# Performance work log

Hardware: AMD Instinct MI355X
Metric: run time of the kernel (lower is better)

## Reference

```python
import jax, jax.numpy as jnp
import numpy as np

DIM = 256
DH = 64            # dim_head
HEADS = DIM // DH  # 4
WH = WW = 8        # window size
EPS = 1e-5


def setup_inputs() -> dict:
    key = jax.random.key(0)
    k1, k2, k3 = jax.random.split(key, 3)
    x = jax.random.normal(k1, (4, DIM, 256, 256), dtype=jnp.float32)
    Wqkv = jax.random.normal(k2, (3 * DIM, DIM), dtype=jnp.float32) * (DIM ** -0.5)
    Wout = jax.random.normal(k3, (DIM, DIM), dtype=jnp.float32) * (DIM ** -0.5)
    gamma = jnp.ones((DIM,), dtype=jnp.float32)
    beta = jnp.zeros((DIM,), dtype=jnp.float32)
    return {"x": x, "gamma": gamma, "beta": beta, "Wqkv": Wqkv, "Wout": Wout}


def _to_windows(t, B, nh, nw):
    # (B, nh*WH, nw*WW, HEADS*DH) -> (B, nh, nw, HEADS, WH*WW, DH)
    t = t.reshape(B, nh, WH, nw, WW, HEADS, DH)
    t = t.transpose(0, 1, 3, 5, 2, 4, 6)
    return t.reshape(B, nh, nw, HEADS, WH * WW, DH)


def reference(x, gamma, beta, Wqkv, Wout):
    B, C, H, W = x.shape
    residual = x
    xh = x.transpose(0, 2, 3, 1)  # (B, H, W, C)
    # LayerNorm over channel dim
    mu = jnp.mean(xh, axis=-1, keepdims=True)
    var = jnp.mean(jnp.square(xh - mu), axis=-1, keepdims=True)
    xn = (xh - mu) * jax.lax.rsqrt(var + EPS) * gamma + beta
    nh, nw = H // WH, W // WW
    qkv = jnp.einsum('bhwc,fc->bhwf', xn, Wqkv)  # (B,H,W,3C)
    q, k, v = jnp.split(qkv, 3, axis=-1)
    q = _to_windows(q, B, nh, nw)
    k = _to_windows(k, B, nh, nw)
    v = _to_windows(v, B, nh, nw)
    scale = DH ** -0.5
    scores = jnp.einsum('bnmhqd,bnmhkd->bnmhqk', q, k) * scale  # 64x64 per window
    attn = jax.nn.softmax(scores, axis=-1)
    o = jnp.einsum('bnmhqk,bnmhkd->bnmhqd', attn, v)
    # merge windows back: (B,nh,nw,HEADS,WH*WW,DH) -> (B,H,W,C)
    o = o.reshape(B, nh, nw, HEADS, WH, WW, DH)
    o = o.transpose(0, 1, 4, 2, 5, 3, 6).reshape(B, H, W, C)
    o = jnp.einsum('bhwc,fc->bhwf', o, Wout)
    return o.transpose(0, 3, 1, 2) + residual
```

## Files before the change

kernel.cpp:

```cpp
#include <hip/hip_runtime.h>
#include <hip/hip_bf16.h>

typedef __attribute__((ext_vector_type(8))) short short8;
typedef __attribute__((ext_vector_type(4))) float floatx4;
typedef __attribute__((ext_vector_type(2))) float floatx2;
typedef __attribute__((ext_vector_type(4))) unsigned short ushort4v;

#define DEVI static __device__ __forceinline__

DEVI unsigned short f2bf(float f) {
  union { __hip_bfloat16 b; unsigned short u; } v;
  v.b = __float2bfloat16(f);
  return v.u;
}
DEVI float bf2f(unsigned short h) { return __uint_as_float(((unsigned int)h) << 16); }

DEVI int ridx2(int c, int t) { return c * 128 + (t ^ ((c & 7) << 3)); }
DEVI int xnaddr(int row, int chunk) { return row * 256 + (((chunk) ^ (row & 7)) << 3); }

DEVI short8 wpfrag(const unsigned short* __restrict__ wbf, int rb, int kc, int lane) {
  return *(const short8*)&wbf[(((size_t)rb * 8 + kc) * 64 + lane) * 8];
}

__global__ void wconv(const float* __restrict__ wqkv, const float* __restrict__ wout,
                      unsigned short* __restrict__ wbf) {
  int cl = blockIdx.x * 256 + threadIdx.x;
  int lane = cl & 63;
  int rbkc = cl >> 6;
  int kc = rbkc & 7;
  int rb = rbkc >> 3;
  int g = lane >> 4, l15 = lane & 15;
  const float* src = (rb < 48) ? wqkv : wout;
  int row = (rb < 48) ? rb * 16 + l15 : (rb - 48) * 16 + l15;
#pragma unroll
  for (int h = 0; h < 2; ++h)
#pragma unroll
    for (int e = 0; e < 4; ++e)
      wbf[(size_t)cl * 8 + h * 4 + e] = f2bf(src[row * 256 + kc * 32 + h * 16 + g * 4 + e]);
}

__global__ __launch_bounds__(512, 2) void k1a_qkv(
    const float* __restrict__ x, const float* __restrict__ gamma,
    const float* __restrict__ beta, const unsigned short* __restrict__ wbf,
    unsigned short* __restrict__ frag) {
  __shared__ __align__(16) unsigned short sx[128 * 256];
  __shared__ floatx2 psum[4][128];

  const int tid = threadIdx.x;
  const int lane = tid & 63;
  const int wv = tid >> 6;
  const int g = lane >> 4;
  const int l15 = lane & 15;

  const int id = ((blockIdx.x & 7) << 8) + (blockIdx.x >> 3);
  const int b = id >> 9;
  const int wy = (id >> 4) & 31;
  const int wxp = id & 15;
  const size_t xbase = ((size_t)b << 24) + (size_t)(wy * 8) * 256 + (size_t)(wxp * 16);

#pragma unroll
  for (int it = 0; it < 16; ++it) {
    int s = it * 512 + tid;
    int c = s >> 5, i = (s >> 2) & 7, j4 = s & 3;
    floatx4 v = *(const floatx4*)(x + xbase + (size_t)c * 65536 + i * 256 + j4 * 4);
    ushort4v u;
    u.x = f2bf(v.x); u.y = f2bf(v.y); u.z = f2bf(v.z); u.w = f2bf(v.w);
    *(ushort4v*)&sx[ridx2(c, i * 16 + j4 * 4)] = u;
  }
  __syncthreads();

  const int t = tid & 127;
  const int q = tid >> 7;
  unsigned int xr[32];
  float s1 = 0.f, s2 = 0.f;
#pragma unroll
  for (int cc = 0; cc < 32; ++cc) {
    unsigned int u0 = sx[ridx2(q * 64 + 2 * cc, t)];
    unsigned int u1 = sx[ridx2(q * 64 + 2 * cc + 1, t)];
    xr[cc] = u0 | (u1 << 16);
    float a = __uint_as_float(u0 << 16);
    float c2 = __uint_as_float(u1 << 16);
    s1 += a + c2;
    s2 = fmaf(a, a, s2); s2 = fmaf(c2, c2, s2);
  }
  { floatx2 p; p.x = s1; p.y = s2; psum[q][t] = p; }
  __syncthreads();

  float S1 = 0.f, S2 = 0.f;
#pragma unroll
  for (int p = 0; p < 4; ++p) { floatx2 pp = psum[p][t]; S1 += pp.x; S2 += pp.y; }
  const float mu = S1 * (1.f / 256.f);
  const float rstd = rsqrtf(S2 * (1.f / 256.f) - mu * mu + 1e-5f);

#pragma unroll
  for (int kk = 0; kk < 2; ++kk) {
    int kc = q * 2 + kk;
#pragma unroll
    for (int gc = 0; gc < 4; ++gc) {
      short8 s8;
#pragma unroll
      for (int hf = 0; hf < 2; ++hf)
#pragma unroll
        for (int e = 0; e < 4; ++e) {
          int lc = kk * 32 + hf * 16 + gc * 4 + e;
          int c = q * 64 + lc;
          unsigned int u = xr[lc >> 1];
          float xv = __uint_as_float((lc & 1) ? (u & 0xffff0000u) : (u << 16));
          float val = (xv - mu) * rstd * gamma[c] + beta[c];
          s8[hf * 4 + e] = (short)f2bf(val);
        }
      *(short8*)&sx[xnaddr(t, kc * 4 + gc)] = s8;
    }
  }
  __syncthreads();

  auto ldsfrag = [&](int row, int kc) -> short8 {
    return *(const short8*)&sx[xnaddr(row, kc * 4 + g)];
  };

  const int head = wv >> 1;
  const int win = wv & 1;
  auto srow = [&](int tl) { return (((tl) >> 3) << 4) + win * 8 + ((tl) & 7); };

  unsigned short* fr = frag + ((size_t)(id * 8 + wv) * 24) * 512 + (size_t)lane * 8;

#pragma unroll
  for (int qk = 0; qk < 2; ++qk) {
    floatx4 acc[4][4] = {};
    const int rbq = qk * 16 + head * 4;
#pragma unroll
    for (int kh = 0; kh < 2; ++kh) {
      short8 wreg[4][4];
#pragma unroll
      for (int kk = 0; kk < 4; ++kk)
#pragma unroll
        for (int mt = 0; mt < 4; ++mt)
          wreg[kk][mt] = wpfrag(wbf, rbq + mt, kh * 4 + kk, lane);
#pragma unroll
      for (int kk = 0; kk < 4; ++kk) {
        int kc = kh * 4 + kk;
        short8 Bv[4];
#pragma unroll
        for (int nt = 0; nt < 4; ++nt) Bv[nt] = ldsfrag(srow(nt * 16 + l15), kc);
#pragma unroll
        for (int mt = 0; mt < 4; ++mt)
#pragma unroll
          for (int nt = 0; nt < 4; ++nt)
            acc[mt][nt] = __builtin_amdgcn_mfma_f32_16x16x32_bf16(wreg[kk][mt], Bv[nt], acc[mt][nt], 0, 0, 0);
      }
    }
#pragma unroll
    for (int nt = 0; nt < 4; ++nt)
#pragma unroll
      for (int ks = 0; ks < 2; ++ks) {
        short8 f;
#pragma unroll
        for (int e = 0; e < 4; ++e) {
          f[e]     = (short)f2bf(acc[2 * ks][nt][e]);
          f[4 + e] = (short)f2bf(acc[2 * ks + 1][nt][e]);
        }
        *(short8*)&fr[(size_t)(qk * 8 + nt * 2 + ks) * 512] = f;
      }
  }

  {
    floatx4 acc[4][4] = {};
#pragma unroll
    for (int kh = 0; kh < 2; ++kh) {
      short8 wreg[4][4];
#pragma unroll
      for (int kk = 0; kk < 4; ++kk)
#pragma unroll
        for (int nt = 0; nt < 4; ++nt)
          wreg[kk][nt] = wpfrag(wbf, 32 + head * 4 + nt, kh * 4 + kk, lane);
#pragma unroll
      for (int kk = 0; kk < 4; ++kk) {
        int kc = kh * 4 + kk;
        short8 Av[4];
#pragma unroll
        for (int mt = 0; mt < 4; ++mt) Av[mt] = ldsfrag(srow(mt * 16 + l15), kc);
#pragma unroll
        for (int mt = 0; mt < 4; ++mt)
#pragma unroll
          for (int nt = 0; nt < 4; ++nt)
            acc[mt][nt] = __builtin_amdgcn_mfma_f32_16x16x32_bf16(Av[mt], wreg[kk][nt], acc[mt][nt], 0, 0, 0);
      }
    }
#pragma unroll
    for (int nt = 0; nt < 4; ++nt)
#pragma unroll
      for (int ks = 0; ks < 2; ++ks) {
        short8 f;
#pragma unroll
        for (int e = 0; e < 4; ++e) {
          f[e]     = (short)f2bf(acc[2 * ks][nt][e]);
          f[4 + e] = (short)f2bf(acc[2 * ks + 1][nt][e]);
        }
        *(short8*)&fr[(size_t)(16 + nt * 2 + ks) * 512] = f;
      }
  }
}

__global__ __launch_bounds__(256, 1) void k1b_attn(
    const unsigned short* __restrict__ frag, unsigned short* __restrict__ o_scr) {
  const int tid = threadIdx.x;
  const int lane = tid & 63;
  const int head = tid >> 6;
  const int g = lane >> 4;
  const int l15 = lane & 15;

  const int id = ((blockIdx.x & 7) << 8) + (blockIdx.x >> 3);
  const int b = id >> 9;
  const int wy = (id >> 4) & 31;
  const int wxp = id & 15;

  const float CEXP = 0.125f * 1.44269504088896f;

#pragma unroll 1
  for (int win = 0; win < 2; ++win) {
    const unsigned short* fr =
        frag + ((size_t)(id * 8 + head * 2 + win) * 24) * 512 + (size_t)lane * 8;

    short8 qkf[2][4][2];
#pragma unroll
    for (int qk = 0; qk < 2; ++qk)
#pragma unroll
      for (int nt = 0; nt < 4; ++nt)
#pragma unroll
        for (int ks = 0; ks < 2; ++ks)
          qkf[qk][nt][ks] = *(const short8*)&fr[(size_t)(qk * 8 + nt * 2 + ks) * 512];

    short8 pf[4][2];
#pragma unroll
    for (int nts = 0; nts < 4; ++nts) {
      floatx4 sac[4] = {};
#pragma unroll
      for (int ks = 0; ks < 2; ++ks)
#pragma unroll
        for (int mts = 0; mts < 4; ++mts)
          sac[mts] = __builtin_amdgcn_mfma_f32_16x16x32_bf16(qkf[1][mts][ks], qkf[0][nts][ks], sac[mts], 0, 0, 0);

      float m = sac[0][0];
#pragma unroll
      for (int mts = 0; mts < 4; ++mts)
#pragma unroll
        for (int r = 0; r < 4; ++r) m = fmaxf(m, sac[mts][r]);
      m = fmaxf(m, __shfl_xor(m, 16));
      m = fmaxf(m, __shfl_xor(m, 32));
      float sum = 0.f;
#pragma unroll
      for (int mts = 0; mts < 4; ++mts)
#pragma unroll
        for (int r = 0; r < 4; ++r) {
          float p = __builtin_amdgcn_exp2f((sac[mts][r] - m) * CEXP);
          sac[mts][r] = p;
          sum += p;
        }
      sum += __shfl_xor(sum, 16);
      sum += __shfl_xor(sum, 32);
      float inv = __builtin_amdgcn_rcpf(sum);
#pragma unroll
      for (int ks = 0; ks < 2; ++ks) {
        short8 f;
#pragma unroll
        for (int e = 0; e < 4; ++e) {
          f[e]     = (short)f2bf(sac[2 * ks][e] * inv);
          f[4 + e] = (short)f2bf(sac[2 * ks + 1][e] * inv);
        }
        pf[nts][ks] = f;
      }
    }

    short8 vf[4][2];
#pragma unroll
    for (int nt = 0; nt < 4; ++nt)
#pragma unroll
      for (int ks = 0; ks < 2; ++ks)
        vf[nt][ks] = *(const short8*)&fr[(size_t)(16 + nt * 2 + ks) * 512];

    floatx4 oa2[4][4];
#pragma unroll
    for (int dt = 0; dt < 4; ++dt)
#pragma unroll
      for (int ntq = 0; ntq < 4; ++ntq) oa2[dt][ntq] = floatx4{0.f, 0.f, 0.f, 0.f};
#pragma unroll
    for (int ks = 0; ks < 2; ++ks)
#pragma unroll
      for (int dt = 0; dt < 4; ++dt)
#pragma unroll
        for (int ntq = 0; ntq < 4; ++ntq)
          oa2[dt][ntq] = __builtin_amdgcn_mfma_f32_16x16x32_bf16(vf[dt][ks], pf[ntq][ks], oa2[dt][ntq], 0, 0, 0);

#pragma unroll
    for (int dtp = 0; dtp < 2; ++dtp)
#pragma unroll
      for (int ntq = 0; ntq < 4; ++ntq) {
        int tq = ntq * 16 + l15;
        size_t orow = ((size_t)b * 256 + wy * 8 + (tq >> 3)) * 256 + wxp * 16 + win * 8 + (tq & 7);
        short8 o8;
#pragma unroll
        for (int r = 0; r < 4; ++r) {
          o8[r]     = (short)f2bf(oa2[2 * dtp][ntq][r]);
          o8[4 + r] = (short)f2bf(oa2[2 * dtp + 1][ntq][r]);
        }
        *(short8*)&o_scr[orow * 256 + head * 64 + dtp * 32 + g * 8] = o8;
      }
  }
}

__global__ __launch_bounds__(512, 2) void k2_proj(
    const unsigned short* __restrict__ o_scr, const float* __restrict__ x,
    const unsigned short* __restrict__ wbf, float* __restrict__ out) {
  __shared__ __align__(16) unsigned short sx[128 * 256];

  const int tid = threadIdx.x;
  const int lane = tid & 63;
  const int wv = tid >> 6;
  const int g = lane >> 4;
  const int l15 = lane & 15;

  const int b = blockIdx.x >> 8;
  const int h = blockIdx.x & 255;

  auto ldsfrag = [&](int row, int kc) -> short8 {
    return *(const short8*)&sx[xnaddr(row, kc * 4 + g)];
  };

#pragma unroll
  for (int hf = 0; hf < 2; ++hf) {
    const size_t obase = (((size_t)b * 256 + h) * 256 + hf * 128) * 256;
#pragma unroll
    for (int it = 0; it < 8; ++it) {
      int s = it * 512 + tid;
      int tl = s >> 5, cid = s & 31;
      short8 v = *(const short8*)&o_scr[obase + tl * 256 + cid * 8];
      *(short8*)&sx[tl * 256 + ((cid ^ (tl & 7)) << 3)] = v;
    }
    __syncthreads();

    floatx4 fa[8][2] = {};
#pragma unroll
    for (int kc = 0; kc < 8; ++kc) {
      short8 Atok[8], Bw[2];
#pragma unroll
      for (int nt = 0; nt < 8; ++nt) Atok[nt] = ldsfrag(nt * 16 + l15, kc);
#pragma unroll
      for (int mt = 0; mt < 2; ++mt)
        Bw[mt] = wpfrag(wbf, 48 + wv * 2 + mt, kc, lane);
#pragma unroll
      for (int nt = 0; nt < 8; ++nt)
#pragma unroll
        for (int mt = 0; mt < 2; ++mt)
          fa[nt][mt] = __builtin_amdgcn_mfma_f32_16x16x32_bf16(Atok[nt], Bw[mt], fa[nt][mt], 0, 0, 0);
    }

#pragma unroll
    for (int nt = 0; nt < 8; ++nt)
#pragma unroll
      for (int mt = 0; mt < 2; ++mt) {
        int co = wv * 32 + mt * 16 + l15;
        size_t addr = (((size_t)(b * 256 + co)) << 16) + (size_t)h * 256 +
                      hf * 128 + nt * 16 + 4 * g;
        floatx4 xv = *(const floatx4*)(x + addr);
        floatx4 o;
#pragma unroll
        for (int r = 0; r < 4; ++r) o[r] = fa[nt][mt][r] + xv[r];
        *(floatx4*)(out + addr) = o;
      }
    __syncthreads();
  }
}

__global__ __launch_bounds__(512, 2) void fused_fallback(
    const float* __restrict__ x, const float* __restrict__ gamma,
    const float* __restrict__ beta, const unsigned short* __restrict__ wbf,
    float* __restrict__ out) {
  __shared__ __align__(16) unsigned short sres[256 * 128];
  __shared__ __align__(16) unsigned short sxn[128 * 256];

  const int tid = threadIdx.x;
  const int lane = tid & 63;
  const int wv = tid >> 6;
  const int g = lane >> 4;
  const int l15 = lane & 15;

  const int id = ((blockIdx.x & 7) << 8) + (blockIdx.x >> 3);
  const int b = id >> 9;
  const int wy = (id >> 4) & 31;
  const int wxp = id & 15;
  const size_t xbase = ((size_t)b << 24) + (size_t)(wy * 8) * 256 + (size_t)(wxp * 16);

#pragma unroll
  for (int it = 0; it < 16; ++it) {
    int s = it * 512 + tid;
    int c = s >> 5, i = (s >> 2) & 7, j4 = s & 3;
    floatx4 v = *(const floatx4*)(x + xbase + (size_t)c * 65536 + i * 256 + j4 * 4);
    ushort4v u;
    u.x = f2bf(v.x); u.y = f2bf(v.y); u.z = f2bf(v.z); u.w = f2bf(v.w);
    *(ushort4v*)&sres[ridx2(c, i * 16 + j4 * 4)] = u;
  }
  __syncthreads();

  const int t = tid & 127;
  const int q = tid >> 7;
  float s1 = 0.f, s2 = 0.f;
#pragma unroll 8
  for (int cc = 0; cc < 64; ++cc) {
    float xv = bf2f(sres[ridx2(q * 64 + cc, t)]);
    s1 += xv; s2 += xv * xv;
  }
  { floatx2 p; p.x = s1; p.y = s2; ((floatx2*)sxn)[q * 128 + t] = p; }
  __syncthreads();

  float S1 = 0.f, S2 = 0.f;
#pragma unroll
  for (int p = 0; p < 4; ++p) {
    floatx2 pp = ((const floatx2*)sxn)[p * 128 + t];
    S1 += pp.x; S2 += pp.y;
  }
  const float mu = S1 * (1.f / 256.f);
  const float rstd = rsqrtf(S2 * (1.f / 256.f) - mu * mu + 1e-5f);
  __syncthreads();

#pragma unroll
  for (int kk = 0; kk < 2; ++kk) {
    int kc = q * 2 + kk;
#pragma unroll
    for (int gc = 0; gc < 4; ++gc) {
      short8 s8;
#pragma unroll
      for (int hf = 0; hf < 2; ++hf)
#pragma unroll
        for (int e = 0; e < 4; ++e) {
          int c = kc * 32 + hf * 16 + gc * 4 + e;
          float xv = bf2f(sres[ridx2(c, t)]);
          float val = (xv - mu) * rstd * gamma[c] + beta[c];
          s8[hf * 4 + e] = (short)f2bf(val);
        }
      *(short8*)&sxn[xnaddr(t, kc * 4 + gc)] = s8;
    }
  }
  __syncthreads();

  auto ldsfrag = [&](int row, int kc) -> short8 {
    return *(const short8*)&sxn[xnaddr(row, kc * 4 + g)];
  };

  const int head = wv >> 1;
  const int win = wv & 1;
  auto srow = [&](int tl) { return (((tl) >> 3) << 4) + win * 8 + ((tl) & 7); };

  short8 qkf[2][4][2];
#pragma unroll
  for (int qk = 0; qk < 2; ++qk) {
    floatx4 acc[4][4] = {};
    const int rbq = qk * 16 + head * 4;
#pragma unroll
    for (int kc = 0; kc < 8; ++kc) {
      short8 Bv[4], Av[4];
#pragma unroll
      for (int nt = 0; nt < 4; ++nt) Bv[nt] = ldsfrag(srow(nt * 16 + l15), kc);
#pragma unroll
      for (int mt = 0; mt < 4; ++mt)
        Av[mt] = wpfrag(wbf, rbq + mt, kc, lane);
#pragma unroll
      for (int mt = 0; mt < 4; ++mt)
#pragma unroll
        for (int nt = 0; nt < 4; ++nt)
          acc[mt][nt] = __builtin_amdgcn_mfma_f32_16x16x32_bf16(Av[mt], Bv[nt], acc[mt][nt], 0, 0, 0);
    }
#pragma unroll
    for (int nt = 0; nt < 4; ++nt)
#pragma unroll
      for (int ks = 0; ks < 2; ++ks) {
        short8 f;
#pragma unroll
        for (int e = 0; e < 4; ++e) {
          f[e]     = (short)f2bf(acc[2 * ks][nt][e]);
          f[4 + e] = (short)f2bf(acc[2 * ks + 1][nt][e]);
        }
        qkf[qk][nt][ks] = f;
      }
  }

  floatx4 sa[4][4] = {};
#pragma unroll
  for (int ks = 0; ks < 2; ++ks)
#pragma unroll
    for (int mts = 0; mts < 4; ++mts)
#pragma unroll
      for (int nts = 0; nts < 4; ++nts)
        sa[mts][nts] = __builtin_amdgcn_mfma_f32_16x16x32_bf16(qkf[1][mts][ks], qkf[0][nts][ks], sa[mts][nts], 0, 0, 0);

  short8 pf[4][2];
  const float CEXP = 0.125f * 1.44269504088896f;
#pragma unroll
  for (int nts = 0; nts < 4; ++nts) {
    float m = sa[0][nts][0];
#pragma unroll
    for (int mts = 0; mts < 4; ++mts)
#pragma unroll
      for (int r = 0; r < 4; ++r) m = fmaxf(m, sa[mts][nts][r]);
    m = fmaxf(m, __shfl_xor(m, 16));
    m = fmaxf(m, __shfl_xor(m, 32));
    float sum = 0.f;
#pragma unroll
    for (int mts = 0; mts < 4; ++mts)
#pragma unroll
      for (int r = 0; r < 4; ++r) {
        float p = __builtin_amdgcn_exp2f((sa[mts][nts][r] - m) * CEXP);
        sa[mts][nts][r] = p;
        sum += p;
      }
    sum += __shfl_xor(sum, 16);
    sum += __shfl_xor(sum, 32);
    float inv = __builtin_amdgcn_rcpf(sum);
#pragma unroll
    for (int ks = 0; ks < 2; ++ks) {
      short8 f;
#pragma unroll
      for (int e = 0; e < 4; ++e) {
        f[e]     = (short)f2bf(sa[2 * ks][nts][e] * inv);
        f[4 + e] = (short)f2bf(sa[2 * ks + 1][nts][e] * inv);
      }
      pf[nts][ks] = f;
    }
  }

  short8 vf[4][2];
  {
    floatx4 acc[4][4] = {};
#pragma unroll
    for (int kc = 0; kc < 8; ++kc) {
      short8 Av[4], Bv[4];
#pragma unroll
      for (int mt = 0; mt < 4; ++mt) Av[mt] = ldsfrag(srow(mt * 16 + l15), kc);
#pragma unroll
      for (int nt = 0; nt < 4; ++nt)
        Bv[nt] = wpfrag(wbf, 32 + head * 4 + nt, kc, lane);
#pragma unroll
      for (int mt = 0; mt < 4; ++mt)
#pragma unroll
        for (int nt = 0; nt < 4; ++nt)
          acc[mt][nt] = __builtin_amdgcn_mfma_f32_16x16x32_bf16(Av[mt], Bv[nt], acc[mt][nt], 0, 0, 0);
    }
#pragma unroll
    for (int nt = 0; nt < 4; ++nt)
#pragma unroll
      for (int ks = 0; ks < 2; ++ks) {
        short8 f;
#pragma unroll
        for (int e = 0; e < 4; ++e) {
          f[e]     = (short)f2bf(acc[2 * ks][nt][e]);
          f[4 + e] = (short)f2bf(acc[2 * ks + 1][nt][e]);
        }
        vf[nt][ks] = f;
      }
  }

  floatx4 oa[4][4] = {};
#pragma unroll
  for (int ks = 0; ks < 2; ++ks)
#pragma unroll
    for (int ntq = 0; ntq < 4; ++ntq)
#pragma unroll
      for (int dt = 0; dt < 4; ++dt)
        oa[ntq][dt] = __builtin_amdgcn_mfma_f32_16x16x32_bf16(pf[ntq][ks], vf[dt][ks], oa[ntq][dt], 0, 0, 0);

  __syncthreads();

#pragma unroll
  for (int ntq = 0; ntq < 4; ++ntq)
#pragma unroll
    for (int dt = 0; dt < 4; ++dt) {
      int c = head * 64 + dt * 16 + l15;
      int kc = c >> 5, hf = (c >> 4) & 1, gc = (c >> 2) & 3, e = c & 3;
#pragma unroll
      for (int r = 0; r < 4; ++r) {
        int tq = ntq * 16 + 4 * g + r;
        int sr = srow(tq);
        sxn[sr * 256 + (((kc * 4 + gc) ^ (sr & 7)) << 3) + hf * 4 + e] =
            f2bf(oa[ntq][dt][r]);
      }
    }
  __syncthreads();

  floatx4 fa[2][8] = {};
#pragma unroll
  for (int kc = 0; kc < 8; ++kc) {
    short8 Bv[8], Av[2];
#pragma unroll
    for (int nt = 0; nt < 8; ++nt) Bv[nt] = ldsfrag(nt * 16 + l15, kc);
#pragma unroll
    for (int mt = 0; mt < 2; ++mt)
      Av[mt] = wpfrag(wbf, 48 + wv * 2 + mt, kc, lane);
#pragma unroll
    for (int mt = 0; mt < 2; ++mt)
#pragma unroll
      for (int nt = 0; nt < 8; ++nt)
        fa[mt][nt] = __builtin_amdgcn_mfma_f32_16x16x32_bf16(Av[mt], Bv[nt], fa[mt][nt], 0, 0, 0);
  }

#pragma unroll
  for (int mt = 0; mt < 2; ++mt)
#pragma unroll
    for (int nt = 0; nt < 8; ++nt)
#pragma unroll
      for (int r = 0; r < 4; ++r) {
        int co = wv * 32 + mt * 16 + 4 * g + r;
        int tt = nt * 16 + l15;
        float val = fa[mt][nt][r] + bf2f(sres[ridx2(co, tt)]);
        out[((size_t)(b * 256 + co) << 16) + (size_t)(wy * 8 + (tt >> 4)) * 256 +
            (wxp * 16 + (tt & 15))] = val;
      }
}

extern "C" void kernel_launch(void* const* d_in, const int* in_sizes, int n_in,
                              void* d_out, int out_size, void* d_ws, size_t ws_size,
                              hipStream_t stream) {
  const float* x     = (const float*)d_in[0];
  const float* gamma = (const float*)d_in[1];
  const float* beta  = (const float*)d_in[2];
  const float* wqkv  = (const float*)d_in[3];
  const float* wout  = (const float*)d_in[4];
  float* out = (float*)d_out;

  unsigned short* wbf   = (unsigned short*)d_ws;
  unsigned short* o_scr = wbf + 262144;
  unsigned short* frag  = o_scr + 67108864;

  const size_t need = 512 * 1024 + (size_t)128 * 1024 * 1024 + (size_t)384 * 1024 * 1024;

  wconv<<<128, 256, 0, stream>>>(wqkv, wout, wbf);
  if (ws_size >= need) {
    k1a_qkv<<<2048, 512, 0, stream>>>(x, gamma, beta, wbf, frag);
    k1b_attn<<<2048, 256, 0, stream>>>(frag, o_scr);
    k2_proj<<<1024, 512, 0, stream>>>(o_scr, x, wbf, out);
  } else {
    fused_fallback<<<2048, 512, 0, stream>>>(x, gamma, beta, wbf, out);
  }
}
```

Baseline: 484.2 us.

## Fuse QKV projection and window attention into one kernel, drop frag scratch

Merges the QKV projection kernel and the attention kernel so that Q, K and V fragments stay in registers and feed softmax and PV directly, with no round trip through a 384MB global scratch buffer. This removes a large write and re-read of intermediate data and one kernel launch. The weight register tile is also halved (kh loop 4x2 instead of 2x4) to offset the register pressure added by holding q/k/v/p fragments, which could still lower occupancy or cause spills under the 512x2 launch bound.

```diff
diff --git a/kernel.cpp b/kernel.cpp
--- a/kernel.cpp
+++ b/kernel.cpp
@@ -39,10 +39,10 @@
       wbf[(size_t)cl * 8 + h * 4 + e] = f2bf(src[row * 256 + kc * 32 + h * 16 + g * 4 + e]);
 }
 
-__global__ __launch_bounds__(512, 2) void k1a_qkv(
+__global__ __launch_bounds__(512, 2) void k1_fused(
     const float* __restrict__ x, const float* __restrict__ gamma,
     const float* __restrict__ beta, const unsigned short* __restrict__ wbf,
-    unsigned short* __restrict__ frag) {
+    unsigned short* __restrict__ o_scr) {
   __shared__ __align__(16) unsigned short sx[128 * 256];
   __shared__ floatx2 psum[4][128];
 
@@ -122,23 +122,24 @@
   const int win = wv & 1;
   auto srow = [&](int tl) { return (((tl) >> 3) << 4) + win * 8 + ((tl) & 7); };
 
-  unsigned short* fr = frag + ((size_t)(id * 8 + wv) * 24) * 512 + (size_t)lane * 8;
-
+  const float CEXP = 0.125f * 1.44269504088896f;
+
+  short8 qf[4][2], kf[4][2];
 #pragma unroll
   for (int qk = 0; qk < 2; ++qk) {
     floatx4 acc[4][4] = {};
     const int rbq = qk * 16 + head * 4;
 #pragma unroll
-    for (int kh = 0; kh < 2; ++kh) {
-      short8 wreg[4][4];
-#pragma unroll
-      for (int kk = 0; kk < 4; ++kk)
+    for (int kh = 0; kh < 4; ++kh) {
+      short8 wreg[2][4];
+#pragma unroll
+      for (int kk = 0; kk < 2; ++kk)
 #pragma unroll
         for (int mt = 0; mt < 4; ++mt)
-          wreg[kk][mt] = wpfrag(wbf, rbq + mt, kh * 4 + kk, lane);
-#pragma unroll
-      for (int kk = 0; kk < 4; ++kk) {
-        int kc = kh * 4 + kk;
+          wreg[kk][mt] = wpfrag(wbf, rbq + mt, kh * 2 + kk, lane);
+#pragma unroll
+      for (int kk = 0; kk < 2; ++kk) {
+        int kc = kh * 2 + kk;
         short8 Bv[4];
 #pragma unroll
         for (int nt = 0; nt < 4; ++nt) Bv[nt] = ldsfrag(srow(nt * 16 + l15), kc);
@@ -159,23 +160,65 @@
           f[e]     = (short)f2bf(acc[2 * ks][nt][e]);
           f[4 + e] = (short)f2bf(acc[2 * ks + 1][nt][e]);
         }
-        *(short8*)&fr[(size_t)(qk * 8 + nt * 2 + ks) * 512] = f;
-      }
-  }
-
+        if (qk == 0) qf[nt][ks] = f; else kf[nt][ks] = f;
+      }
+  }
+
+  short8 pf[4][2];
+#pragma unroll
+  for (int nts = 0; nts < 4; ++nts) {
+    floatx4 sac[4] = {};
+#pragma unroll
+    for (int ks = 0; ks < 2; ++ks)
+#pragma unroll
+      for (int mts = 0; mts < 4; ++mts)
+        sac[mts] = __builtin_amdgcn_mfma_f32_16x16x32_bf16(kf[mts][ks], qf[nts][ks], sac[mts], 0, 0, 0);
+
+    float m = sac[0][0];
+#pragma unroll
+    for (int mts = 0; mts < 4; ++mts)
+#pragma unroll
+      for (int r = 0; r < 4; ++r) m = fmaxf(m, sac[mts][r]);
+    m = fmaxf(m, __shfl_xor(m, 16));
+    m = fmaxf(m, __shfl_xor(m, 32));
+    float sum = 0.f;
+#pragma unroll
+    for (int mts = 0; mts < 4; ++mts)
+#pragma unroll
+      for (int r = 0; r < 4; ++r) {
+        float p = __builtin_amdgcn_exp2f((sac[mts][r] - m) * CEXP);
+        sac[mts][r] = p;
+        sum += p;
+      }
+    sum += __shfl_xor(sum, 16);
+    sum += __shfl_xor(sum, 32);
+    float inv = __builtin_amdgcn_rcpf(sum);
+#pragma unroll
+    for (int ks = 0; ks < 2; ++ks) {
+      short8 f;
+#pragma unroll
+      for (int e = 0; e < 4; ++e) {
+        f[e]     = (short)f2bf(sac[2 * ks][e] * inv);
+        f[4 + e] = (short)f2bf(sac[2 * ks + 1][e] * inv);
+      }
+      pf[nts][ks] = f;
+    }
+  }
+
+  short8 vf[4][2];
   {
     floatx4 acc[4][4] = {};
 #pragma unroll
-    for (int kh = 0; kh < 2; ++kh) {
-      short8 wreg[4][4];
-#pragma unroll
-      for (int kk = 0; kk < 4; ++kk)
+    for (int kh = 0; kh < 4; ++kh) {
+      short8 wreg[2][4];
+#pragma unroll
+      for (int kk = 0; kk < 2; ++kk)
 #pragma unroll
         for (int nt = 0; nt < 4; ++nt)
-          wreg[kk][nt] = wpfrag(wbf, 32 + head * 4 + nt, kh * 4 + kk, lane);
-#pragma unroll
-      for (int kk = 0; kk < 4; ++kk) {
-        int kc = kh * 4 + kk;
+          wreg[kk][nt] = wpfrag(wbf, 32 + head * 4 + nt, kh * 2 + kk, lane);
+#pragma unroll
+      for (int kk = 0; kk < 2; ++kk) {
+        int kc = kh * 2 + kk;
         short8 Av[4];
 #pragma unroll
         for (int mt = 0; mt < 4; ++mt) Av[mt] = ldsfrag(srow(mt * 16 + l15), kc);
@@ -196,116 +239,37 @@
           f[e]     = (short)f2bf(acc[2 * ks][nt][e]);
           f[4 + e] = (short)f2bf(acc[2 * ks + 1][nt][e]);
         }
-        *(short8*)&fr[(size_t)(16 + nt * 2 + ks) * 512] = f;
-      }
-  }
-}
-
-__global__ __launch_bounds__(256, 1) void k1b_attn(
-    const unsigned short* __restrict__ frag, unsigned short* __restrict__ o_scr) {
-  const int tid = threadIdx.x;
-  const int lane = tid & 63;
-  const int head = tid >> 6;
-  const int g = lane >> 4;
-  const int l15 = lane & 15;
-
-  const int id = ((blockIdx.x & 7) << 8) + (blockIdx.x >> 3);
-  const int b = id >> 9;
-  const int wy = (id >> 4) & 31;
-  const int wxp = id & 15;
-
-  const float CEXP = 0.125f * 1.44269504088896f;
-
-#pragma unroll 1
-  for (int win = 0; win < 2; ++win) {
-    const unsigned short* fr =
-        frag + ((size_t)(id * 8 + head * 2 + win) * 24) * 512 + (size_t)lane * 8;
-
-    short8 qkf[2][4][2];
-#pragma unroll
-    for (int qk = 0; qk < 2; ++qk)
-#pragma unroll
-      for (int nt = 0; nt < 4; ++nt)
-#pragma unroll
-        for (int ks = 0; ks < 2; ++ks)
-          qkf[qk][nt][ks] = *(const short8*)&fr[(size_t)(qk * 8 + nt * 2 + ks) * 512];
-
-    short8 pf[4][2];
-#pragma unroll
-    for (int nts = 0; nts < 4; ++nts) {
-      floatx4 sac[4] = {};
-#pragma unroll
-      for (int ks = 0; ks < 2; ++ks)
-#pragma unroll
-        for (int mts = 0; mts < 4; ++mts)
-          sac[mts] = __builtin_amdgcn_mfma_f32_16x16x32_bf16(qkf[1][mts][ks], qkf[0][nts][ks], sac[mts], 0, 0, 0);
-
-      float m = sac[0][0];
-#pragma unroll
-      for (int mts = 0; mts < 4; ++mts)
-#pragma unroll
-        for (int r = 0; r < 4; ++r) m = fmaxf(m, sac[mts][r]);
-      m = fmaxf(m, __shfl_xor(m, 16));
-      m = fmaxf(m, __shfl_xor(m, 32));
-      float sum = 0.f;
-#pragma unroll
-      for (int mts = 0; mts < 4; ++mts)
-#pragma unroll
-        for (int r = 0; r < 4; ++r) {
-          float p = __builtin_amdgcn_exp2f((sac[mts][r] - m) * CEXP);
-          sac[mts][r] = p;
-          sum += p;
-        }
-      sum += __shfl_xor(sum, 16);
-      sum += __shfl_xor(sum, 32);
-      float inv = __builtin_amdgcn_rcpf(sum);
-#pragma unroll
-      for (int ks = 0; ks < 2; ++ks) {
-        short8 f;
-#pragma unroll
-        for (int e = 0; e < 4; ++e) {
-          f[e]     = (short)f2bf(sac[2 * ks][e] * inv);
-          f[4 + e] = (short)f2bf(sac[2 * ks + 1][e] * inv);
-        }
-        pf[nts][ks] = f;
-      }
-    }
-
-    short8 vf[4][2];
-#pragma unroll
-    for (int nt = 0; nt < 4; ++nt)
-#pragma unroll
-      for (int ks = 0; ks < 2; ++ks)
-        vf[nt][ks] = *(const short8*)&fr[(size_t)(16 + nt * 2 + ks) * 512];
-
-    floatx4 oa2[4][4];
+        vf[nt][ks] = f;
+      }
+  }
+
+  floatx4 oa2[4][4];
+#pragma unroll
+  for (int dt = 0; dt < 4; ++dt)
+#pragma unroll
+    for (int ntq = 0; ntq < 4; ++ntq) oa2[dt][ntq] = floatx4{0.f, 0.f, 0.f, 0.f};
+#pragma unroll
+  for (int ks = 0; ks < 2; ++ks)
 #pragma unroll
     for (int dt = 0; dt < 4; ++dt)
 #pragma unroll
-      for (int ntq = 0; ntq < 4; ++ntq) oa2[dt][ntq] = floatx4{0.f, 0.f, 0.f, 0.f};
-#pragma unroll
-    for (int ks = 0; ks < 2; ++ks)
-#pragma unroll
-      for (int dt = 0; dt < 4; ++dt)
-#pragma unroll
-        for (int ntq = 0; ntq < 4; ++ntq)
-          oa2[dt][ntq] = __builtin_amdgcn_mfma_f32_16x16x32_bf16(vf[dt][ks], pf[ntq][ks], oa2[dt][ntq], 0, 0, 0);
-
-#pragma unroll
-    for (int dtp = 0; dtp < 2; ++dtp)
-#pragma unroll
-      for (int ntq = 0; ntq < 4; ++ntq) {
-        int tq = ntq * 16 + l15;
-        size_t orow = ((size_t)b * 256 + wy * 8 + (tq >> 3)) * 256 + wxp * 16 + win * 8 + (tq & 7);
-        short8 o8;
-#pragma unroll
-        for (int r = 0; r < 4; ++r) {
-          o8[r]     = (short)f2bf(oa2[2 * dtp][ntq][r]);
-          o8[4 + r] = (short)f2bf(oa2[2 * dtp + 1][ntq][r]);
-        }
-        *(short8*)&o_scr[orow * 256 + head * 64 + dtp * 32 + g * 8] = o8;
-      }
-  }
+      for (int ntq = 0; ntq < 4; ++ntq)
+        oa2[dt][ntq] = __builtin_amdgcn_mfma_f32_16x16x32_bf16(vf[dt][ks], pf[ntq][ks], oa2[dt][ntq], 0, 0, 0);
+
+#pragma unroll
+  for (int dtp = 0; dtp < 2; ++dtp)
+#pragma unroll
+    for (int ntq = 0; ntq < 4; ++ntq) {
+      int tq = ntq * 16 + l15;
+      size_t orow = ((size_t)b * 256 + wy * 8 + (tq >> 3)) * 256 + wxp * 16 + win * 8 + (tq & 7);
+      short8 o8;
+#pragma unroll
+      for (int r = 0; r < 4; ++r) {
+        o8[r]     = (short)f2bf(oa2[2 * dtp][ntq][r]);
+        o8[4 + r] = (short)f2bf(oa2[2 * dtp + 1][ntq][r]);
+      }
+      *(short8*)&o_scr[orow * 256 + head * 64 + dtp * 32 + g * 8] = o8;
+    }
 }
 
 __global__ __launch_bounds__(512, 2) void k2_proj(
@@ -627,14 +591,12 @@
 
   unsigned short* wbf   = (unsigned short*)d_ws;
   unsigned short* o_scr = wbf + 262144;
-  unsigned short* frag  = o_scr + 67108864;
-
-  const size_t need = 512 * 1024 + (size_t)128 * 1024 * 1024 + (size_t)384 * 1024 * 1024;
+
+  const size_t need = 512 * 1024 + (size_t)128 * 1024 * 1024;
 
   wconv<<<128, 256, 0, stream>>>(wqkv, wout, wbf);
   if (ws_size >= need) {
-    k1a_qkv<<<2048, 512, 0, stream>>>(x, gamma, beta, wbf, frag);
-    k1b_attn<<<2048, 256, 0, stream>>>(frag, o_scr);
+    k1_fused<<<2048, 512, 0, stream>>>(x, gamma, beta, wbf, o_scr);
     k2_proj<<<1024, 512, 0, stream>>>(o_scr, x, wbf, out);
   } else {
     fused_fallback<<<2048, 512, 0, stream>>>(x, gamma, beta, wbf, out);
```

After: 480.4 us. No clear change (-0.8%).
